# Optimization experiments

Hardware: AMD Instinct MI355X
Metric: run time of the kernel (lower is better)

## Reference

```python
import jax, jax.numpy as jnp
import numpy as np

S = 4        # patch stride
G = 4        # offset groups
C = 1024     # token channels = 64*4*4
CG = C // G  # 256 channels per group


def _conv2d(x, w, b, pad, groups=1):
    y = jax.lax.conv_general_dilated(x, w, (1, 1), [(pad, pad), (pad, pad)],
                                     dimension_numbers=('NCHW', 'OIHW', 'NCHW'),
                                     feature_group_count=groups)
    return y if b is None else y + b.reshape(1, -1, 1, 1)


def _ln_c(x, g, b, eps=1e-5):
    # LayerNormProxy: LayerNorm over the channel dim of NCHW
    mu = jnp.mean(x, axis=1, keepdims=True)
    var = jnp.mean((x - mu) ** 2, axis=1, keepdims=True)
    return (x - mu) * jax.lax.rsqrt(var + eps) * g.reshape(1, -1, 1, 1) + b.reshape(1, -1, 1, 1)


def _l2norm(x, axis, eps=1e-12):
    n = jnp.sqrt(jnp.sum(x * x, axis=axis, keepdims=True))
    return x / jnp.maximum(n, eps)


def _gs_nearest(img, grid):
    # F.grid_sample(mode='nearest', padding_mode='zeros', align_corners=True)
    B, Cc, H, W = img.shape
    x = (grid[..., 0] + 1.0) * 0.5 * (W - 1)
    y = (grid[..., 1] + 1.0) * 0.5 * (H - 1)
    xi = jnp.round(x).astype(jnp.int32)
    yi = jnp.round(y).astype(jnp.int32)
    valid = ((xi >= 0) & (xi < W) & (yi >= 0) & (yi < H)).astype(img.dtype)
    xc = jnp.clip(xi, 0, W - 1)
    yc = jnp.clip(yi, 0, H - 1)
    vals = jax.vmap(lambda im, yy, xx: im[:, yy, xx])(img, yc, xc)  # (B,C,Hg,Wg)
    return vals * valid[:, None]


def _gs_bilinear(img, grid):
    # F.grid_sample(mode='bilinear', padding_mode='zeros', align_corners=True)
    B, Cc, H, W = img.shape
    x = (grid[..., 0] + 1.0) * 0.5 * (W - 1)
    y = (grid[..., 1] + 1.0) * 0.5 * (H - 1)
    x0 = jnp.floor(x)
    y0 = jnp.floor(y)
    wx1 = x - x0
    wy1 = y - y0

    def tap(yf, xf, wgt):
        xi = xf.astype(jnp.int32)
        yi = yf.astype(jnp.int32)
        valid = ((xf >= 0) & (xf < W) & (yf >= 0) & (yf < H)).astype(img.dtype)
        xc = jnp.clip(xi, 0, W - 1)
        yc = jnp.clip(yi, 0, H - 1)
        v = jax.vmap(lambda im, yy, xx: im[:, yy, xx])(img, yc, xc)
        return v * (valid * wgt)[:, None]

    return (tap(y0, x0, (1 - wy1) * (1 - wx1)) + tap(y0, x0 + 1, (1 - wy1) * wx1)
            + tap(y0 + 1, x0, wy1 * (1 - wx1)) + tap(y0 + 1, x0 + 1, wy1 * wx1))


def _unfold_s(x):
    # F.unfold(kernel=(S,S), stride=S): (n,c,h,w) -> (n, c*S*S, (h/S)*(w/S))
    n, c, h, w = x.shape
    x = x.reshape(n, c, h // S, S, w // S, S).transpose(0, 1, 3, 5, 2, 4)
    return x.reshape(n, c * S * S, (h // S) * (w // S))


def _fold_s(x, h, w):
    # F.fold, inverse of _unfold_s (no overlap since kernel == stride)
    n, cl, L = x.shape
    c = cl // (S * S)
    x = x.reshape(n, c, S, S, h // S, w // S).transpose(0, 1, 4, 2, 5, 3)
    return x.reshape(n, c, h, w)


def _ref_points(Hk, Wk, dtype):
    ry = (jnp.linspace(0.5, Hk - 0.5, Hk, dtype=dtype) / Hk) * 2.0 - 1.0
    rx = (jnp.linspace(0.5, Wk - 0.5, Wk, dtype=dtype) / Wk) * 2.0 - 1.0
    gy, gx = jnp.meshgrid(ry, rx, indexing='ij')
    return jnp.stack([gy, gx], -1)  # (Hk, Wk, 2) ordered (y, x)


def _forward(curr_feat, index_feat_set_s1, anchor_feat, s1, s2, s3, location_feat,
             fusion_w, fusion_b, to_dw_w, to_dw_b, to_ln_w, to_ln_b, to_pw_w):
    n, c, h, w = curr_feat.shape
    t = s1.shape[1]
    H4, W4 = h // S, w // S
    feat_len = c * S * S          # 1024
    feat_num = H4 * W4

    # build normalized flow grid (x, y) from location map
    gf = location_feat.reshape(n, t, 2, H4, W4).transpose(0, 1, 3, 4, 2)
    gx = 2.0 * gf[..., 0] / max(W4 - 1, 1) - 1.0
    gy = 2.0 * gf[..., 1] / max(H4 - 1, 1) - 1.0
    grid = jnp.stack([gx, gy], -1).reshape(n * t, H4, W4, 2)

    o1 = _gs_nearest(s1.reshape(n * t, feat_len, H4, W4), grid)
    o2 = _gs_nearest(s2.reshape(n * t, feat_len, H4, W4), grid)
    o3 = _gs_nearest(s3.reshape(n * t, feat_len, H4, W4), grid)
    idx = _gs_nearest(index_feat_set_s1.reshape(n * t, feat_len, H4, W4), grid)

    # index tokens -> (n, feat_num, t, C), L2-normalized over C
    idx = idx.reshape(n, t, feat_len, feat_num).transpose(0, 3, 1, 2)
    idx = _l2norm(idx, 3)

    # current-frame tokens -> (n, feat_num, C), L2-normalized
    cf = _unfold_s(curr_feat).transpose(0, 2, 1)
    cf = _l2norm(cf, 2)

    temporal_q = cf.reshape(n, H4, W4, C).transpose(0, 3, 1, 2)                       # (n, C, H4, W4)
    temporal_k = idx.transpose(0, 2, 1, 3).reshape(n * t, H4, W4, C).transpose(0, 3, 1, 2)

    # offset subnetwork (time_offset)
    q_off = jnp.tile(temporal_q.reshape(n * G, CG, H4, W4), (t, 1, 1, 1))            # repeat(t,1,1,1)
    k_off = temporal_k.reshape(n * t * G, CG, H4, W4)
    off = jnp.concatenate([q_off, k_off], axis=1)                                     # (n*t*G, 2*CG, H4, W4)
    o = _conv2d(off, to_dw_w, to_dw_b, 2, groups=CG)
    o = jax.nn.gelu(_ln_c(o, to_ln_w, to_ln_b), approximate=False)
    offset = _conv2d(o, to_pw_w, None, 0)                                             # (n*t*G, 2, Hk, Wk)
    Hk, Wk = offset.shape[2], offset.shape[3]
    orange = jnp.array([1.0 / Hk, 1.0 / Wk], dtype=offset.dtype).reshape(1, 2, 1, 1)
    offset = jnp.tanh(offset) * orange * 2.0                                          # offset_range_factor = 2
    pos = offset.transpose(0, 2, 3, 1) + _ref_points(Hk, Wk, offset.dtype)[None]      # (y, x)
    grid2 = pos[..., ::-1]                                                            # (x, y)

    # deformable sampling of temporal keys, cosine QK attention (max over t)
    tks = _gs_bilinear(temporal_k.reshape(n * t * G, CG, Hk, Wk), grid2)
    tks = tks.reshape(n, t, G, CG, Hk, Wk).transpose(0, 4, 5, 1, 2, 3).reshape(n, Hk * Wk, t, C)
    matrix_index = jnp.einsum('nltc,nlc->nlt', tks, cf)                               # (n, feat_num, t)
    corr_soft = jnp.max(matrix_index, axis=2)
    corr_index = jnp.argmax(matrix_index, axis=2)
    corr_soft_map = _fold_s(jnp.broadcast_to(corr_soft[:, None, :], (n, feat_len, feat_num)), h, w)

    def sample_gather(ox):
        v = _gs_bilinear(ox.reshape(n * t * G, CG, H4, W4), grid2)
        v = v.reshape(n, t, feat_len, feat_num)
        v = jnp.take_along_axis(v, corr_index[:, None, None, :], axis=1)[:, 0]
        return _fold_s(v, h, w)

    f1 = sample_gather(o1)
    f2 = sample_gather(o2)
    f3 = sample_gather(o3)

    out = _conv2d(jnp.concatenate([f1, f2, f3], axis=1), fusion_w, fusion_b, 1)
    out = out * corr_soft_map + anchor_feat
    return out


def setup_inputs() -> dict:
    key = jax.random.key(0)
    ks = jax.random.split(key, 12)
    n, t, h, w, c = 2, 12, 96, 96, 64
    H4, W4 = h // 4, w // 4
    fl = c * 16
    f = lambda k, sh, s=1.0: jax.random.normal(k, sh, dtype=jnp.float32) * s
    return {
        'curr_feat': f(ks[0], (n, c, h, w)),
        'index_feat_set_s1': f(ks[1], (n, t, fl, H4, W4)),
        'anchor_feat': f(ks[2], (n, c, h, w)),
        'sparse_feat_set_s1': f(ks[3], (n, t, fl, H4, W4)),
        'sparse_feat_set_s2': f(ks[4], (n, t, fl, H4, W4)),
        'sparse_feat_set_s3': f(ks[5], (n, t, fl, H4, W4)),
        'location_feat': jax.random.uniform(ks[6], (n, 2 * t, H4, W4), dtype=jnp.float32) * W4,
        'fusion_w': f(ks[7], (64, 192, 3, 3), 0.02),
        'fusion_b': jnp.zeros((64,), jnp.float32),
        'to_dw_w': f(ks[8], (256, 2, 5, 5), 0.05),
        'to_dw_b': jnp.zeros((256,), jnp.float32),
        'to_ln_w': jnp.ones((256,), jnp.float32),
        'to_ln_b': jnp.zeros((256,), jnp.float32),
        'to_pw_w': f(ks[9], (2, 256, 1, 1), 0.05),
    }


def reference(curr_feat, index_feat_set_s1, anchor_feat, sparse_feat_set_s1,
              sparse_feat_set_s2, sparse_feat_set_s3, location_feat,
              fusion_w, fusion_b, to_dw_w, to_dw_b, to_ln_w, to_ln_b, to_pw_w):
    return _forward(curr_feat, index_feat_set_s1, anchor_feat, sparse_feat_set_s1,
                    sparse_feat_set_s2, sparse_feat_set_s3, location_feat,
                    fusion_w, fusion_b, to_dw_w, to_dw_b, to_ln_w, to_ln_b, to_pw_w)
```

## Files before the change

kernel.cpp:

```cpp
#include <hip/hip_runtime.h>
#include <hip/hip_bf16.h>
#include <math.h>

#define NN 2
#define TT 12
#define HH 96
#define WW 96
#define CC 64
#define H4 24
#define W4 24
#define FL 1024
#define FN 576

typedef short short8 __attribute__((ext_vector_type(8)));
typedef float f32x4 __attribute__((ext_vector_type(4)));

__device__ __forceinline__ float u2f(unsigned short u){
  unsigned int x = ((unsigned int)u)<<16; float f; __builtin_memcpy(&f,&x,4); return f;
}
__device__ __forceinline__ unsigned short f2u(float f){
  __hip_bfloat16 b = __float2bfloat16(f); unsigned short u; __builtin_memcpy(&u,&b,2); return u;
}

__global__ void k_map(const float* __restrict__ loc, int* __restrict__ smap){
  int i = blockIdx.x*256 + threadIdx.x;
  if (i >= NN*TT*FN) return;
  int nt = i / FN, pix = i % FN;
  int ni = nt / TT, ti = nt % TT;
  const float* lp = loc + ((size_t)ni*(2*TT) + 2*ti)*FN + pix;
  float vx = lp[0];
  float vy = lp[FN];
  float gx = (2.0f*vx)/23.0f - 1.0f;
  float gy = (2.0f*vy)/23.0f - 1.0f;
  float x = ((gx + 1.0f)*0.5f)*23.0f;
  float y = ((gy + 1.0f)*0.5f)*23.0f;
  int xi = (int)rintf(x);
  int yi = (int)rintf(y);
  bool valid = (xi>=0)&&(xi<W4)&&(yi>=0)&&(yi<H4);
  smap[i] = valid ? (yi*W4+xi) : -1;
}

__global__ void k_part(const float* __restrict__ idxf, float* __restrict__ part){
  int blk = blockIdx.x;
  int nt = blk >> 4, ch0 = (blk & 15)*64;
  int pix = threadIdx.x;
  const float* p = idxf + ((size_t)nt*FL + ch0)*FN + pix;
  float s = 0.f;
  for (int c=0;c<64;c++){ float v = p[(size_t)c*FN]; s += v*v; }
  part[(size_t)blk*FN + pix] = s;
}
__global__ void k_norm(const float* __restrict__ part, float* __restrict__ nrm){
  int i = blockIdx.x*256+threadIdx.x;
  if (i>=NN*TT*FN) return;
  int nt = i/FN, pix = i%FN;
  float s=0.f;
  for (int c=0;c<16;c++) s += part[(size_t)(nt*16+c)*FN + pix];
  nrm[i] = sqrtf(s);
}

__global__ void k_cf(const float* __restrict__ curr, float* __restrict__ cf){
  int blk = blockIdx.x;
  int ni = blk/FN, l = blk%FN;
  int by = l/W4, bx = l%W4;
  int tid = threadIdx.x;
  int ci = tid>>2, sy = tid&3;
  const float* p = curr + (((size_t)ni*CC+ci)*HH + by*4+sy)*WW + bx*4;
  float4 v = *(const float4*)p;
  float s = v.x*v.x+v.y*v.y+v.z*v.z+v.w*v.w;
  __shared__ float red[256];
  red[tid]=s; __syncthreads();
  for(int o=128;o>0;o>>=1){ if(tid<o) red[tid]+=red[tid+o]; __syncthreads(); }
  float r = 1.0f/fmaxf(sqrtf(red[0]),1e-12f);
  float4 o4 = make_float4(v.x*r, v.y*r, v.z*r, v.w*r);
  ((float4*)(cf + (size_t)blk*FL))[tid] = o4;
}

__global__ __launch_bounds__(256) void k_tr_idx(const float* __restrict__ idxf,
    const float* __restrict__ nrm, float* __restrict__ idxT){
  int b = blockIdx.x;
  int cht = b & 15; int b2 = b >> 4;
  int pixt = b2 % 9; int nt = b2 / 9;
  int tid = threadIdx.x;
  __shared__ float t[64][65];
  #pragma unroll
  for (int r=0; r<16; ++r){
    int ch_l = r*4 + (tid>>6), pix_l = tid & 63;
    t[ch_l][pix_l] = idxf[((size_t)nt*FL + cht*64 + ch_l)*FN + pixt*64 + pix_l];
  }
  __syncthreads();
  #pragma unroll
  for (int r=0; r<16; ++r){
    int pix_l = r*4 + (tid>>6), ch_l = tid & 63;
    int gpix = pixt*64 + pix_l;
    float inv = 1.0f/fmaxf(nrm[nt*FN + gpix], 1e-12f);
    idxT[((size_t)nt*FN + gpix)*FL + cht*64 + ch_l] = t[ch_l][pix_l]*inv;
  }
}

__global__ __launch_bounds__(256) void k_tr_s(const float* __restrict__ s1,
    const float* __restrict__ s2, const float* __restrict__ s3,
    unsigned short* __restrict__ sT){
  int b = blockIdx.x;
  int tens = b / 3456; int bb = b % 3456;
  int cht = bb & 15; int b2 = bb >> 4;
  int pixt = b2 % 9; int nt = b2 / 9;
  const float* src = (tens==0)? s1 : (tens==1)? s2 : s3;
  int tid = threadIdx.x;
  __shared__ float t[64][65];
  #pragma unroll
  for (int r=0; r<16; ++r){
    int ch_l = r*4 + (tid>>6), pix_l = tid & 63;
    t[ch_l][pix_l] = src[((size_t)nt*FL + cht*64 + ch_l)*FN + pixt*64 + pix_l];
  }
  __syncthreads();
  #pragma unroll
  for (int r=0; r<16; ++r){
    int pix_l = r*4 + (tid>>6), ch_l = tid & 63;
    int gpix = pixt*64 + pix_l;
    sT[((size_t)(tens*NN*TT + nt)*FN + gpix)*FL + cht*64 + ch_l] = f2u(t[ch_l][pix_l]);
  }
}

__global__ void k_wpack(const float* __restrict__ fw, unsigned short* __restrict__ wp){
  int idx = blockIdx.x*256 + threadIdx.x;
  if (idx >= 9*6*4*64*8) return;
  int j = idx & 7; int t2 = idx >> 3;
  int L = t2 & 63; int t3 = t2 >> 6;
  int ntl = t3 & 3; int t4 = t3 >> 2;
  int kc = t4 % 6; int tap = t4 / 6;
  int dy = tap/3, dx = tap%3;
  int n = ntl*16 + (L & 15);
  int quad = L >> 4;
  int k = kc*32 + quad*8 + j;
  wp[idx] = f2u(fw[((size_t)n*192 + k)*9 + dy*3 + dx]);
}

__global__ __launch_bounds__(256) void k_offnet(
    const float* __restrict__ cf, const float* __restrict__ idxT,
    const int* __restrict__ smap,
    const float* __restrict__ dw_w, const float* __restrict__ dw_b,
    const float* __restrict__ ln_w, const float* __restrict__ ln_b,
    const float* __restrict__ pw_w, float* __restrict__ grid2){
  int i0 = blockIdx.x;
  int xcd = i0 & 7; int kk = i0 >> 3;
  int b = (kk/12)*8 + xcd;
  int y0 = 2*(kk%12);
  int i = threadIdx.x;
  float wA[25], wB[25];
  const float* wp = dw_w + (size_t)i*50;
  #pragma unroll
  for(int k=0;k<25;k++){ wA[k]=wp[k]; wB[k]=wp[25+k]; }
  const float* src; int choff; const int* smrow;
  if (i < 128){
    int n2 = (b>>2)&1, g2 = b&3;
    src = cf + (size_t)n2*FN*FL;
    choff = g2*256 + 2*i;
    smrow = nullptr;
  } else {
    int nk = b/48, tik = (b>>2)%12, gk = b&3;
    int nt = nk*TT + tik;
    src = idxT + (size_t)nt*FN*FL;
    choff = gk*256 + 2*(i-128);
    smrow = smap + nt*FN;
  }
  float acc[2][24];
  #pragma unroll
  for(int x=0;x<24;x++){ acc[0][x]=0.f; acc[1][x]=0.f; }
  for(int r = y0-2; r <= y0+3; ++r){
    if (r < 0 || r >= H4) continue;
    int dy0 = r - y0 + 2;
    int dy1 = dy0 - 1;
    bool u0 = (dy0 < 5), u1 = (dy1 >= 0);
    #pragma unroll
    for(int xx=0; xx<24; ++xx){
      int pixsrc = smrow ? smrow[r*W4+xx] : (r*W4+xx);
      float2 v = make_float2(0.f,0.f);
      if (pixsrc >= 0) v = *(const float2*)(src + (size_t)pixsrc*FL + choff);
      #pragma unroll
      for(int dd=0; dd<5; ++dd){
        int x = xx + 2 - dd;
        if (x>=0 && x<24){
          if (u0) acc[0][x] += v.x*wA[dy0*5+dd] + v.y*wB[dy0*5+dd];
          if (u1) acc[1][x] += v.x*wA[dy1*5+dd] + v.y*wB[dy1*5+dd];
        }
      }
    }
  }
  float bias = dw_b[i];
  #pragma unroll
  for(int x=0;x<24;x++){ acc[0][x]+=bias; acc[1][x]+=bias; }
  __shared__ float lds[256*25];
  __shared__ float smean[24], srstd[24];
  float gi = ln_w[i], bi = ln_b[i];
  #pragma unroll
  for(int yy=0; yy<2; ++yy){
    int y = y0 + yy;
    #pragma unroll
    for(int x=0;x<24;x++) lds[i*25+x]=acc[yy][x];
    __syncthreads();
    if (i<24){
      float s=0.f,s2=0.f;
      for(int j=0;j<256;j++){ float v=lds[j*25+i]; s+=v; s2+=v*v; }
      float mean = s*(1.0f/256.0f);
      float var = s2*(1.0f/256.0f) - mean*mean;
      smean[i]=mean; srstd[i]=rsqrtf(var+1e-5f);
    }
    __syncthreads();
    #pragma unroll
    for(int x=0;x<24;x++){
      float v = (acc[yy][x]-smean[x])*srstd[x]*gi + bi;
      float ge = 0.5f*v*(1.0f + erff(v*0.70710678118654752f));
      lds[i*25+x] = ge;
    }
    __syncthreads();
    if (i<24){
      float d0=0.f,d1=0.f;
      for(int j=0;j<256;j++){ float v=lds[j*25+i]; d0 += v*pw_w[j]; d1 += v*pw_w[256+j]; }
      float off0 = tanhf(d0)*(2.0f/24.0f);
      float off1 = tanhf(d1)*(2.0f/24.0f);
      float ry = (((float)y + 0.5f)/24.0f)*2.0f - 1.0f;
      float rx = (((float)i + 0.5f)/24.0f)*2.0f - 1.0f;
      float posy = off0 + ry, posx = off1 + rx;
      float px = ((posx + 1.0f)*0.5f)*23.0f;
      float py = ((posy + 1.0f)*0.5f)*23.0f;
      *(float2*)(grid2 + ((size_t)b*FN + y*W4 + i)*2) = make_float2(px, py);
    }
    __syncthreads();
  }
}

__global__ __launch_bounds__(256) void k_corr(const float* __restrict__ cf,
    const float* __restrict__ idxT, const int* __restrict__ smap,
    const float* __restrict__ grid2,
    float* __restrict__ cors, int* __restrict__ cori){
  int i0 = blockIdx.x;
  int band = i0 & 7; int k0 = i0 >> 3;
  int ni = k0/72; int r0 = k0%72;
  int y = band*3 + r0/24; int xx = r0%24;
  int l = y*24 + xx;
  int blk = ni*FN + l;
  int tid = threadIdx.x;
  int g = tid>>6;
  float4 cfv = ((const float4*)(cf + (size_t)blk*FL))[tid];
  __shared__ float red[4];
  float best=-3.4e38f; int bidx=0;
  for(int ti=0; ti<TT; ++ti){
    int nt = ni*TT+ti;
    float2 gr = *(const float2*)(grid2 + ((size_t)(ni*48 + ti*4 + g)*FN + l)*2);
    float x0f = floorf(gr.x), y0f = floorf(gr.y);
    float wx = gr.x - x0f, wy = gr.y - y0f;
    float partial = 0.f;
    #pragma unroll
    for(int tap=0; tap<4; ++tap){
      float xf = x0f + (float)(tap&1);
      float yf = y0f + (float)(tap>>1);
      float w = ((tap&1)? wx : 1.f-wx) * ((tap>>1)? wy : 1.f-wy);
      if (xf>=0.f && xf<24.f && yf>=0.f && yf<24.f){
        int xi=(int)xf, yi=(int)yf;
        int sp2 = smap[nt*FN + yi*W4+xi];
        if (sp2 >= 0){
          float4 tv = ((const float4*)(idxT + (size_t)(nt*FN + sp2)*FL))[tid];
          partial += w*(tv.x*cfv.x + tv.y*cfv.y + tv.z*cfv.z + tv.w*cfv.w);
        }
      }
    }
    for(int o=32;o>0;o>>=1) partial += __shfl_down(partial, o, 64);
    if ((tid&63)==0) red[tid>>6]=partial;
    __syncthreads();
    if (tid==0){
      float s = red[0]+red[1]+red[2]+red[3];
      if (s > best){ best=s; bidx=ti; }
    }
    __syncthreads();
  }
  if (tid==0){ cors[blk]=best; cori[blk]=bidx; }
}

__global__ __launch_bounds__(256) void k_gather(const float* __restrict__ s1,
    const float* __restrict__ s2, const float* __restrict__ s3,
    const unsigned short* __restrict__ sT, int use_t,
    const int* __restrict__ smap, const float* __restrict__ grid2,
    const int* __restrict__ cori, unsigned short* __restrict__ fcat){
  int blk = blockIdx.x; int ni = blk/FN, l = blk%FN;
  int tid = threadIdx.x;
  int g = tid>>6;
  int ts = cori[blk];
  int nt = ni*TT + ts;
  float2 gr = *(const float2*)(grid2 + ((size_t)(ni*48 + ts*4 + g)*FN + l)*2);
  float x0f = floorf(gr.x), y0f = floorf(gr.y);
  float wx = gr.x - x0f, wy = gr.y - y0f;
  int sp[4]; float wt[4];
  #pragma unroll
  for(int tap=0; tap<4; ++tap){
    float xf = x0f + (float)(tap&1), yf = y0f + (float)(tap>>1);
    float w = ((tap&1)? wx : 1.f-wx)*((tap>>1)? wy : 1.f-wy);
    bool v = (xf>=0.f && xf<24.f && yf>=0.f && yf<24.f);
    int xi=(int)xf, yi=(int)yf;
    int pp = v ? smap[nt*FN + yi*W4+xi] : -1;
    sp[tap] = (pp>=0)? pp : 0; wt[tap] = (v && pp>=0)? w : 0.f;
  }
  float a[3][4];
  #pragma unroll
  for(int t2=0;t2<3;t2++){ a[t2][0]=0.f;a[t2][1]=0.f;a[t2][2]=0.f;a[t2][3]=0.f; }
  if (use_t){
    #pragma unroll
    for(int tap=0;tap<4;++tap){
      float w = wt[tap];
      if (w != 0.f){
        #pragma unroll
        for(int t2=0;t2<3;t2++){
          const unsigned short* p = sT + ((size_t)(t2*NN*TT + nt)*FN + sp[tap])*FL + tid*4;
          ushort4 r = *(const ushort4*)p;
          a[t2][0] += w*u2f(r.x); a[t2][1] += w*u2f(r.y);
          a[t2][2] += w*u2f(r.z); a[t2][3] += w*u2f(r.w);
        }
      }
    }
  } else {
    size_t chbase = ((size_t)nt*FL + tid*4)*FN;
    const float* sa[3] = { s1+chbase, s2+chbase, s3+chbase };
    #pragma unroll
    for(int t2=0;t2<3;t2++){
      #pragma unroll
      for(int tap=0;tap<4;++tap){
        float w = wt[tap];
        if (w != 0.f){
          const float* p = sa[t2] + sp[tap];
          a[t2][0] += w*p[0]; a[t2][1] += w*p[FN];
          a[t2][2] += w*p[2*FN]; a[t2][3] += w*p[3*FN];
        }
      }
    }
  }
  __shared__ float ldsv[3*16*65];
  #pragma unroll
  for(int t2=0;t2<3;t2++){
    #pragma unroll
    for(int k=0;k<4;k++){
      int cl = tid*4 + k;
      ldsv[t2*1040 + (cl&15)*65 + (cl>>4)] = a[t2][k];
    }
  }
  __syncthreads();
  int by = l/W4, bx = l%W4;
  int subpix = tid>>4, j = tid&15;
  int sy = subpix>>2, sx = subpix&3;
  unsigned short tmp[12];
  #pragma unroll
  for(int kk=0;kk<12;kk++){
    int ch = j*12+kk; int t2 = ch>>6; int ci = ch&63;
    tmp[kk] = f2u(ldsv[t2*1040 + subpix*65 + ci]);
  }
  unsigned short* dst = fcat + (((size_t)(ni*HH + by*4+sy))*WW + bx*4+sx)*192 + j*12;
  uint2* d2 = (uint2*)dst;
  d2[0] = make_uint2((unsigned)tmp[0] | ((unsigned)tmp[1]<<16), (unsigned)tmp[2] | ((unsigned)tmp[3]<<16));
  d2[1] = make_uint2((unsigned)tmp[4] | ((unsigned)tmp[5]<<16), (unsigned)tmp[6] | ((unsigned)tmp[7]<<16));
  d2[2] = make_uint2((unsigned)tmp[8] | ((unsigned)tmp[9]<<16), (unsigned)tmp[10]| ((unsigned)tmp[11]<<16));
}

__global__ __launch_bounds__(256) void k_fusion_mfma(
    const unsigned short* __restrict__ fcat, const unsigned short* __restrict__ wpk,
    const float* __restrict__ fb, const float* __restrict__ cors,
    const float* __restrict__ anchor, float* __restrict__ out){
  int b = blockIdx.x;
  int ni = b/288; int rem = b%288; int y = rem/3, xb = rem%3; int x0 = xb*32;
  int tid = threadIdx.x;
  __shared__ __align__(16) char sbuf[40960];
  unsigned short* aT = (unsigned short*)sbuf;
  for (int i = tid; i < 3*34*48; i += 256){
    int ch4 = i % 48; int t2 = i / 48;
    int xx = t2 % 34; int rr = t2 / 34;
    int row = y - 1 + rr, sx = x0 - 1 + xx;
    uint2 v = make_uint2(0u, 0u);
    if (row >= 0 && row < HH && sx >= 0 && sx < WW)
      v = *(const uint2*)(fcat + (((size_t)(ni*HH + row))*WW + sx)*192 + ch4*4);
    *(uint2*)(aT + ((size_t)rr*34 + xx)*200 + ch4*4) = v;
  }
  __syncthreads();
  int wv = tid>>6, lane = tid&63;
  int mt = wv&1, np = wv>>1;
  int m = lane&15, quad = lane>>4;
  f32x4 c0 = {0.f,0.f,0.f,0.f}, c1 = {0.f,0.f,0.f,0.f};
  for (int tap=0; tap<9; ++tap){
    int dy = tap/3, dx = tap%3;
    const unsigned short* arow = aT + ((size_t)dy*34 + mt*16 + m + dx)*200 + quad*8;
    #pragma unroll
    for (int kc=0; kc<6; ++kc){
      short8 af = *(const short8*)(arow + kc*32);
      const unsigned short* bp = wpk + (size_t)((tap*6+kc)*4 + np*2)*512 + lane*8;
      short8 b0 = *(const short8*)(bp);
      short8 b1 = *(const short8*)(bp + 512);
      c0 = __builtin_amdgcn_mfma_f32_16x16x32_bf16(af, b0, c0, 0, 0, 0);
      c1 = __builtin_amdgcn_mfma_f32_16x16x32_bf16(af, b1, c1, 0, 0, 0);
    }
  }
  __syncthreads();
  float* oT = (float*)sbuf;
  #pragma unroll
  for (int r=0; r<4; ++r){
    int xl = mt*16 + quad*4 + r;
    oT[xl*65 + np*32 + m]      = c0[r];
    oT[xl*65 + np*32 + 16 + m] = c1[r];
  }
  __syncthreads();
  for (int i = tid; i < 2048; i += 256){
    int co = i >> 5, xl = i & 31;
    int x = x0 + xl;
    float csm = cors[ni*FN + (y>>2)*W4 + (x>>2)];
    size_t oidx = ((size_t)(ni*CC + co)*HH + y)*WW + x;
    out[oidx] = (oT[xl*65 + co] + fb[co])*csm + anchor[oidx];
  }
}

extern "C" void kernel_launch(void* const* d_in, const int* in_sizes, int n_in,
                              void* d_out, int out_size, void* d_ws, size_t ws_size,
                              hipStream_t stream) {
  const float* curr   = (const float*)d_in[0];
  const float* idxf   = (const float*)d_in[1];
  const float* anchor = (const float*)d_in[2];
  const float* s1 = (const float*)d_in[3];
  const float* s2 = (const float*)d_in[4];
  const float* s3 = (const float*)d_in[5];
  const float* loc = (const float*)d_in[6];
  const float* fw  = (const float*)d_in[7];
  const float* fb  = (const float*)d_in[8];
  const float* dww = (const float*)d_in[9];
  const float* dwb = (const float*)d_in[10];
  const float* lnw = (const float*)d_in[11];
  const float* lnb = (const float*)d_in[12];
  const float* pww = (const float*)d_in[13];
  char* ws = (char*)d_ws;
  const size_t MB = 1024*1024;
  int*            smap  = (int*)           (ws + 0);
  float*          nrm   = (float*)         (ws + 1*MB);
  float*          part  = (float*)         (ws + 2*MB);
  float*          cf    = (float*)         (ws + 3*MB);
  float*          idxT  = (float*)         (ws + 8*MB);
  float*          grid2 = (float*)         (ws + 62*MB);
  float*          cors  = (float*)         (ws + 63*MB);
  int*            cori  = (int*)           (ws + 63*MB + 8192);
  unsigned short* fcat  = (unsigned short*)(ws + 64*MB);
  unsigned short* wpk   = (unsigned short*)(ws + 71*MB);
  unsigned short* sT    = (unsigned short*)(ws + 72*MB);
  int use_t = (ws_size >= (size_t)(72*MB) + 84934656u) ? 1 : 0;
  float* out = (float*)d_out;

  k_map   <<<54,    256, 0, stream>>>(loc, smap);
  k_part  <<<384,   576, 0, stream>>>(idxf, part);
  k_norm  <<<54,    256, 0, stream>>>(part, nrm);
  k_cf    <<<1152,  256, 0, stream>>>(curr, cf);
  k_tr_idx<<<3456,  256, 0, stream>>>(idxf, nrm, idxT);
  if (use_t)
    k_tr_s<<<10368, 256, 0, stream>>>(s1, s2, s3, sT);
  k_wpack <<<432,   256, 0, stream>>>(fw, wpk);
  k_offnet<<<1152,  256, 0, stream>>>(cf, idxT, smap, dww, dwb, lnw, lnb, pww, grid2);
  k_corr  <<<1152,  256, 0, stream>>>(cf, idxT, smap, grid2, cors, cori);
  k_gather<<<1152,  256, 0, stream>>>(s1, s2, s3, sT, use_t, smap, grid2, cori, fcat);
  k_fusion_mfma<<<576, 256, 0, stream>>>(fcat, wpk, fb, cors, anchor, out);
}
```

Measured before the change: 558.2 us.

## Parallelize offnet LayerNorm and pointwise reductions across 240 threads

```diff
diff --git a/kernel.cpp b/kernel.cpp
--- a/kernel.cpp
+++ b/kernel.cpp
@@ -135,7 +135,7 @@
   wp[idx] = f2u(fw[((size_t)n*192 + k)*9 + dy*3 + dx]);
 }
 
-__global__ __launch_bounds__(256) void k_offnet(
+__global__ __launch_bounds__(256, 2) void k_offnet(
     const float* __restrict__ cf, const float* __restrict__ idxT,
     const int* __restrict__ smap,
     const float* __restrict__ dw_w, const float* __restrict__ dw_b,
@@ -146,6 +146,14 @@
   int b = (kk/12)*8 + xcd;
   int y0 = 2*(kk%12);
   int i = threadIdx.x;
+
+  __shared__ float smat[256][25];
+  __shared__ float spart[2][10][24];
+  __shared__ float sstat[2][24];
+  __shared__ float pw0s[256], pw1s[256];
+
+  pw0s[i] = pw_w[i]; pw1s[i] = pw_w[256+i];
+
   float wA[25], wB[25];
   const float* wp = dw_w + (size_t)i*50;
   #pragma unroll
@@ -166,22 +174,22 @@
   float acc[2][24];
   #pragma unroll
   for(int x=0;x<24;x++){ acc[0][x]=0.f; acc[1][x]=0.f; }
-  for(int r = y0-2; r <= y0+3; ++r){
-    if (r < 0 || r >= H4) continue;
-    int dy0 = r - y0 + 2;
-    int dy1 = dy0 - 1;
-    bool u0 = (dy0 < 5), u1 = (dy1 >= 0);
-    #pragma unroll
-    for(int xx=0; xx<24; ++xx){
-      int pixsrc = smrow ? smrow[r*W4+xx] : (r*W4+xx);
-      float2 v = make_float2(0.f,0.f);
-      if (pixsrc >= 0) v = *(const float2*)(src + (size_t)pixsrc*FL + choff);
+  #pragma unroll
+  for(int rr=0; rr<6; ++rr){
+    int r = y0 - 2 + rr;
+    if (r >= 0 && r < H4){
       #pragma unroll
-      for(int dd=0; dd<5; ++dd){
-        int x = xx + 2 - dd;
-        if (x>=0 && x<24){
-          if (u0) acc[0][x] += v.x*wA[dy0*5+dd] + v.y*wB[dy0*5+dd];
-          if (u1) acc[1][x] += v.x*wA[dy1*5+dd] + v.y*wB[dy1*5+dd];
+      for(int xx=0; xx<24; ++xx){
+        int pixsrc = smrow ? smrow[r*W4+xx] : (r*W4+xx);
+        float2 v = make_float2(0.f,0.f);
+        if (pixsrc >= 0) v = *(const float2*)(src + (size_t)pixsrc*FL + choff);
+        #pragma unroll
+        for(int dd=0; dd<5; ++dd){
+          int x = xx + 2 - dd;
+          if (x>=0 && x<24){
+            if (rr < 5) acc[0][x] += v.x*wA[rr*5+dd]     + v.y*wB[rr*5+dd];
+            if (rr >= 1) acc[1][x] += v.x*wA[(rr-1)*5+dd] + v.y*wB[(rr-1)*5+dd];
+          }
         }
       }
     }
@@ -189,33 +197,49 @@
   float bias = dw_b[i];
   #pragma unroll
   for(int x=0;x<24;x++){ acc[0][x]+=bias; acc[1][x]+=bias; }
-  __shared__ float lds[256*25];
-  __shared__ float smean[24], srstd[24];
   float gi = ln_w[i], bi = ln_b[i];
-  #pragma unroll
+
   for(int yy=0; yy<2; ++yy){
     int y = y0 + yy;
     #pragma unroll
-    for(int x=0;x<24;x++) lds[i*25+x]=acc[yy][x];
-    __syncthreads();
-    if (i<24){
+    for(int x=0;x<24;x++) smat[i][x] = acc[yy][x];
+    __syncthreads();
+    if (i < 240){
+      int x = i % 24, seg = i / 24;
+      int j0 = seg*26, j1 = (seg==9)? 256 : (j0+26);
+      float s=0.f, s2=0.f;
+      for(int j=j0;j<j1;++j){ float v=smat[j][x]; s+=v; s2+=v*v; }
+      spart[0][seg][x]=s; spart[1][seg][x]=s2;
+    }
+    __syncthreads();
+    if (i < 24){
       float s=0.f,s2=0.f;
-      for(int j=0;j<256;j++){ float v=lds[j*25+i]; s+=v; s2+=v*v; }
+      #pragma unroll
+      for(int g2=0;g2<10;g2++){ s+=spart[0][g2][i]; s2+=spart[1][g2][i]; }
       float mean = s*(1.0f/256.0f);
-      float var = s2*(1.0f/256.0f) - mean*mean;
-      smean[i]=mean; srstd[i]=rsqrtf(var+1e-5f);
+      float var  = s2*(1.0f/256.0f) - mean*mean;
+      sstat[0][i]=mean; sstat[1][i]=rsqrtf(var+1e-5f);
     }
     __syncthreads();
     #pragma unroll
     for(int x=0;x<24;x++){
-      float v = (acc[yy][x]-smean[x])*srstd[x]*gi + bi;
+      float v = (acc[yy][x]-sstat[0][x])*sstat[1][x]*gi + bi;
       float ge = 0.5f*v*(1.0f + erff(v*0.70710678118654752f));
-      lds[i*25+x] = ge;
-    }
-    __syncthreads();
-    if (i<24){
+      smat[i][x] = ge;
+    }
+    __syncthreads();
+    if (i < 240){
+      int x = i % 24, seg = i / 24;
+      int j0 = seg*26, j1 = (seg==9)? 256 : (j0+26);
+      float d0=0.f, d1=0.f;
+      for(int j=j0;j<j1;++j){ float v=smat[j][x]; d0+=v*pw0s[j]; d1+=v*pw1s[j]; }
+      spart[0][seg][x]=d0; spart[1][seg][x]=d1;
+    }
+    __syncthreads();
+    if (i < 24){
       float d0=0.f,d1=0.f;
-      for(int j=0;j<256;j++){ float v=lds[j*25+i]; d0 += v*pw_w[j]; d1 += v*pw_w[256+j]; }
+      #pragma unroll
+      for(int g2=0;g2<10;g2++){ d0+=spart[0][g2][i]; d1+=spart[1][g2][i]; }
       float off0 = tanhf(d0)*(2.0f/24.0f);
       float off1 = tanhf(d1)*(2.0f/24.0f);
       float ry = (((float)y + 0.5f)/24.0f)*2.0f - 1.0f;
```

After: 529.9 us. -5.1%, faster.
